# Kernel optimization log

Measured on AMD Instinct MI355X. Metric: run time of the kernel, lower is better.

Reference implementation:

```python
import jax, jax.numpy as jnp
import numpy as np

N = 500_000
E = 16_000_000
G = 5_000
F_IN = 64
DIM = 10


def _mlp(x, W1, b1, W2, b2):
    return jnp.maximum(x @ W1 + b1, 0.0) @ W2 + b2


def setup_inputs() -> dict:
    key = jax.random.key(0)
    ks = jax.random.split(key, 32)
    inp = {
        "h": jax.random.normal(ks[0], (N, F_IN), dtype=jnp.float32),
        "src": jax.random.randint(ks[1], (E,), 0, N, dtype=jnp.int32),
        "dst": jax.random.randint(ks[2], (E,), 0, N, dtype=jnp.int32),
        "node_graph": jnp.sort(jax.random.randint(ks[3], (N,), 0, G, dtype=jnp.int32)),
    }
    k = 4
    for i in range(1, 6):
        d_in = F_IN if i == 1 else DIM
        inp[f"W1_{i}"] = jax.random.normal(ks[k], (d_in, DIM), dtype=jnp.float32) * 0.1; k += 1
        inp[f"b1_{i}"] = jnp.zeros((DIM,), dtype=jnp.float32)
        inp[f"W2_{i}"] = jax.random.normal(ks[k], (DIM, DIM), dtype=jnp.float32) * 0.1; k += 1
        inp[f"b2_{i}"] = jnp.zeros((DIM,), dtype=jnp.float32)
        inp[f"l_{i}"] = jax.random.normal(ks[k], (DIM, 1), dtype=jnp.float32) * 0.1; k += 1
    return inp


def reference(h, src, dst, node_graph,
              W1_1, b1_1, W2_1, b2_1, l_1,
              W1_2, b1_2, W2_2, b2_2, l_2,
              W1_3, b1_3, W2_3, b2_3, l_3,
              W1_4, b1_4, W2_4, b2_4, l_4,
              W1_5, b1_5, W2_5, b2_5, l_5):
    # GINConv with eps=0: out = MLP(h + sum_{j in N(i)} h_j), then outer ReLU
    def gin(x, W1, b1, W2, b2):
        agg = jax.ops.segment_sum(x[src], dst, num_segments=N)
        return jnp.maximum(_mlp(x + agg, W1, b1, W2, b2), 0.0)

    x1 = gin(h, W1_1, b1_1, W2_1, b2_1)
    x2 = gin(x1, W1_2, b1_2, W2_2, b2_2)
    x3 = gin(x2, W1_3, b1_3, W2_3, b2_3)
    x4 = gin(x3, W1_4, b1_4, W2_4, b2_4)
    x5 = gin(x4, W1_5, b1_5, W2_5, b2_5)

    counts = jax.ops.segment_sum(jnp.ones((N,), dtype=jnp.float32), node_graph, num_segments=G)
    counts = jnp.maximum(counts, 1.0)[:, None]  # [G,1]

    def mean_nodes(x):
        return jax.ops.segment_sum(x, node_graph, num_segments=G) / counts

    s = (mean_nodes(x1) @ l_1 + mean_nodes(x2) @ l_2 + mean_nodes(x3) @ l_3
         + mean_nodes(x4) @ l_4 + mean_nodes(x5) @ l_5)  # [G,1]
    return jax.nn.sigmoid(s)
```

## Files before the change

kernel.cpp:

```cpp
#include <hip/hip_runtime.h>


#define NBLK 256

__device__ __forceinline__ unsigned short f2bf(float f) {
    unsigned b = __float_as_uint(f);
    b += 0x7fffu + ((b >> 16) & 1u);
    return (unsigned short)(b >> 16);
}
__device__ __forceinline__ float bflo(unsigned u) { return __uint_as_float(u << 16); }
__device__ __forceinline__ float bfhi(unsigned u) { return __uint_as_float(u & 0xffff0000u); }

__global__ void k1_hw1_bf16(const float* __restrict__ h, const float* __restrict__ W1,
                            unsigned* __restrict__ y, int N) {
    __shared__ float sW[640];
    for (int i = threadIdx.x; i < 640; i += blockDim.x) sW[i] = W1[i];
    __syncthreads();
    int n = blockIdx.x * blockDim.x + threadIdx.x;
    if (n >= N) return;
    const float* hr = h + (size_t)n * 64;
    float acc[10];
#pragma unroll
    for (int j = 0; j < 10; j++) acc[j] = 0.f;
#pragma unroll 4
    for (int k = 0; k < 64; k += 4) {
        float4 hv = *(const float4*)(hr + k);
#pragma unroll
        for (int j = 0; j < 10; j++) {
            acc[j] += hv.x * sW[(k + 0) * 10 + j];
            acc[j] += hv.y * sW[(k + 1) * 10 + j];
            acc[j] += hv.z * sW[(k + 2) * 10 + j];
            acc[j] += hv.w * sW[(k + 3) * 10 + j];
        }
    }
    unsigned r0 = (unsigned)f2bf(acc[0]) | ((unsigned)f2bf(acc[1]) << 16);
    unsigned r1 = (unsigned)f2bf(acc[2]) | ((unsigned)f2bf(acc[3]) << 16);
    unsigned r2 = (unsigned)f2bf(acc[4]) | ((unsigned)f2bf(acc[5]) << 16);
    unsigned r3 = (unsigned)f2bf(acc[6]) | ((unsigned)f2bf(acc[7]) << 16);
    unsigned r4 = (unsigned)f2bf(acc[8]) | ((unsigned)f2bf(acc[9]) << 16);
    unsigned* yr = y + (size_t)n * 8;
    *(uint4*)yr = make_uint4(r0, r1, r2, r3);
    yr[4] = r4;
}

__global__ void k1_hw1_f32(const float* __restrict__ h, const float* __restrict__ W1,
                           float* __restrict__ y, int N) {
    __shared__ float sW[640];
    for (int i = threadIdx.x; i < 640; i += blockDim.x) sW[i] = W1[i];
    __syncthreads();
    int n = blockIdx.x * blockDim.x + threadIdx.x;
    if (n >= N) return;
    const float* hr = h + (size_t)n * 64;
    float acc[10];
#pragma unroll
    for (int j = 0; j < 10; j++) acc[j] = 0.f;
#pragma unroll 4
    for (int k = 0; k < 64; k += 4) {
        float4 hv = *(const float4*)(hr + k);
#pragma unroll
        for (int j = 0; j < 10; j++) {
            acc[j] += hv.x * sW[(k + 0) * 10 + j];
            acc[j] += hv.y * sW[(k + 1) * 10 + j];
            acc[j] += hv.z * sW[(k + 2) * 10 + j];
            acc[j] += hv.w * sW[(k + 3) * 10 + j];
        }
    }
    float* yr = y + (size_t)n * 16;
#pragma unroll
    for (int j = 0; j < 10; j++) yr[j] = acc[j];
}

__global__ __launch_bounds__(1024) void k_cnt(
        const int* __restrict__ dst, unsigned* __restrict__ gcnt, int E) {
    __shared__ unsigned h[512];
    int t = threadIdx.x;
    if (t < 512) h[t] = 0;
    __syncthreads();
    int per = (E + NBLK - 1) / NBLK;
    int beg = blockIdx.x * per;
    int end = beg + per; if (end > E) end = E;
    for (int e = beg + t; e < end; e += 1024)
        atomicAdd(&h[(unsigned)dst[e] >> 10], 1u);
    __syncthreads();
    if (t < 512) gcnt[blockIdx.x * 512 + t] = h[t];
}

__global__ __launch_bounds__(NBLK) void k_scan2(
        const unsigned* __restrict__ gcnt, unsigned* __restrict__ gbase,
        unsigned* __restrict__ btot) {
    __shared__ unsigned s[NBLK];
    int b = blockIdx.x;
    int t = threadIdx.x;
    unsigned v = gcnt[t * 512 + b];
    s[t] = v;
    __syncthreads();
    for (int off = 1; off < NBLK; off <<= 1) {
        unsigned u = (t >= off) ? s[t - off] : 0u;
        __syncthreads();
        s[t] += u;
        __syncthreads();
    }
    gbase[t * 512 + b] = s[t] - v;
    if (t == NBLK - 1) btot[b] = s[t];
}

__global__ void k_bscan(const unsigned* __restrict__ btot,
                        unsigned* __restrict__ bbase, int B) {
    __shared__ unsigned s[512];
    int t = threadIdx.x;
    unsigned v = (t < B) ? btot[t] : 0u;
    s[t] = v;
    __syncthreads();
    for (int off = 1; off < 512; off <<= 1) {
        unsigned u = (t >= off) ? s[t - off] : 0u;
        __syncthreads();
        s[t] += u;
        __syncthreads();
    }
    if (t < B) bbase[t] = s[t] - v;
    if (t == B - 1) bbase[B] = s[t];
}

__global__ __launch_bounds__(1024) void k_scatter(
        const int* __restrict__ src, const int* __restrict__ dst,
        const unsigned* __restrict__ bbase, const unsigned* __restrict__ gbase,
        unsigned* __restrict__ pairs, int E) {
    __shared__ unsigned cur[512];
    int t = threadIdx.x;
    if (t < 512) cur[t] = bbase[t] + gbase[blockIdx.x * 512 + t];
    __syncthreads();
    int per = (E + NBLK - 1) / NBLK;
    int beg = blockIdx.x * per;
    int end = beg + per; if (end > E) end = E;
    for (int e = beg + t; e < end; e += 1024) {
        unsigned d = (unsigned)dst[e];
        unsigned pos = atomicAdd(&cur[d >> 10], 1u);
        pairs[pos] = ((unsigned)src[e] << 10) | (d & 1023u);
    }
}

__global__ __launch_bounds__(1024) void k_p2(
        const unsigned* __restrict__ pairs, const unsigned* __restrict__ bbase,
        unsigned* __restrict__ edges, unsigned* __restrict__ row_start,
        int N, int B, int E, int packed) {
    __shared__ unsigned cnt[1024], scn[1024], cur[1024];
    int t = threadIdx.x, b = blockIdx.x;
    unsigned beg = bbase[b], end = bbase[b + 1];
    cnt[t] = 0;
    __syncthreads();
    for (unsigned e = beg + t; e < end; e += 1024)
        atomicAdd(&cnt[pairs[e] & 1023u], 1u);
    __syncthreads();
    unsigned v = cnt[t];
    scn[t] = v;
    __syncthreads();
    for (int off = 1; off < 1024; off <<= 1) {
        unsigned u = (t >= off) ? scn[t - off] : 0u;
        __syncthreads();
        scn[t] += u;
        __syncthreads();
    }
    unsigned excl = scn[t] - v;
    int node = (b << 10) + t;
    if (node < N) row_start[node] = beg + excl;
    if (b == B - 1 && t == 0) row_start[N] = (unsigned)E;
    cur[t] = beg + excl;
    __syncthreads();
    for (unsigned e = beg + t; e < end; e += 1024) {
        unsigned pv = pairs[e];
        unsigned pos = atomicAdd(&cur[pv & 1023u], 1u);
        edges[pos] = packed ? pv : (pv >> 10);
    }
}

__global__ __launch_bounds__(256, 4) void k_layerQ(
        const unsigned* __restrict__ yin, unsigned* __restrict__ yout,
        const unsigned* __restrict__ row_start, const unsigned* __restrict__ edges,
        const float* __restrict__ b1, const float* __restrict__ W2,
        const float* __restrict__ b2, const float* __restrict__ l,
        const float* __restrict__ W1n,
        const int* __restrict__ node_graph, float* __restrict__ gacc,
        int N, int last) {
    __shared__ float sW2[100], sW1[100], sb1[10], sb2[10], sl[10];
    int t = threadIdx.x;
    if (t < 100) sW2[t] = W2[t];
    if (!last && t >= 128 && t < 228) sW1[t - 128] = W1n[t - 128];
    if (t < 10) { sb1[t] = b1[t]; sb2[t] = b2[t]; sl[t] = l[t]; }
    __syncthreads();
    int q = t & 3;
    int n = blockIdx.x * 64 + (t >> 2);
    bool valid = n < N;
    int nc = valid ? n : (N - 1);

    float acc[10];
#pragma unroll
    for (int j = 0; j < 10; j++) acc[j] = 0.f;

    unsigned beg = 0, end = 0;
    if (valid) { beg = row_start[n]; end = row_start[n + 1]; }
    unsigned e = beg + (unsigned)q;
    bool have = e < end;
    unsigned sNext = 0;
    if (have) sNext = edges[e];
    while (have) {
        unsigned sCur = sNext;
        unsigned en = e + 4;
        bool hn = en < end;
        if (hn) sNext = edges[en];
        const unsigned* p = yin + (size_t)sCur * 8;
        uint4 a0 = *(const uint4*)p;
        unsigned b0 = p[4];
        acc[0] += bflo(a0.x); acc[1] += bfhi(a0.x);
        acc[2] += bflo(a0.y); acc[3] += bfhi(a0.y);
        acc[4] += bflo(a0.z); acc[5] += bfhi(a0.z);
        acc[6] += bflo(a0.w); acc[7] += bfhi(a0.w);
        acc[8] += bflo(b0);   acc[9] += bfhi(b0);
        e = en; have = hn;
    }

#pragma unroll
    for (int j = 0; j < 10; j++) acc[j] += __shfl_xor(acc[j], 1);
#pragma unroll
    for (int j = 0; j < 10; j++) acc[j] += __shfl_xor(acc[j], 2);

    const unsigned* yr = yin + (size_t)nc * 8;
    uint4 qa = *(const uint4*)yr;
    unsigned q4 = yr[4];
    acc[0] += bflo(qa.x); acc[1] += bfhi(qa.x);
    acc[2] += bflo(qa.y); acc[3] += bfhi(qa.y);
    acc[4] += bflo(qa.z); acc[5] += bfhi(qa.z);
    acc[6] += bflo(qa.w); acc[7] += bfhi(qa.w);
    acc[8] += bflo(q4);   acc[9] += bfhi(q4);

    float z[10], x[10];
#pragma unroll
    for (int j = 0; j < 10; j++) {
        float v = acc[j] + sb1[j];
        z[j] = v > 0.f ? v : 0.f;
    }
#pragma unroll
    for (int j = 0; j < 10; j++) {
        float v = sb2[j];
#pragma unroll
        for (int k = 0; k < 10; k++) v += z[k] * sW2[k * 10 + j];
        x[j] = v > 0.f ? v : 0.f;
    }
    float p = 0.f;
#pragma unroll
    for (int j = 0; j < 10; j++) p += x[j] * sl[j];
    if (!valid) p = 0.f;
    int g = node_graph[nc];

    int g0 = __shfl(g, 0);
    if (__all(g == g0)) {
#pragma unroll
        for (int off = 32; off > 0; off >>= 1) p += __shfl_down(p, off);
        if ((t & 63) == 0) unsafeAtomicAdd(&gacc[g0], p * 0.25f);
    } else {
        if (valid && q == 0) unsafeAtomicAdd(&gacc[g], p);
    }

    if (!last && valid && q == 0) {
        float yn[10];
#pragma unroll
        for (int j = 0; j < 10; j++) {
            float v = 0.f;
#pragma unroll
            for (int k = 0; k < 10; k++) v += x[k] * sW1[k * 10 + j];
            yn[j] = v;
        }
        unsigned r0 = (unsigned)f2bf(yn[0]) | ((unsigned)f2bf(yn[1]) << 16);
        unsigned r1 = (unsigned)f2bf(yn[2]) | ((unsigned)f2bf(yn[3]) << 16);
        unsigned r2 = (unsigned)f2bf(yn[4]) | ((unsigned)f2bf(yn[5]) << 16);
        unsigned r3 = (unsigned)f2bf(yn[6]) | ((unsigned)f2bf(yn[7]) << 16);
        unsigned r4 = (unsigned)f2bf(yn[8]) | ((unsigned)f2bf(yn[9]) << 16);
        unsigned* yo = yout + (size_t)n * 8;
        *(uint4*)yo = make_uint4(r0, r1, r2, r3);
        yo[4] = r4;
    }
}

__global__ void k4_final(const float* __restrict__ gacc, const int* __restrict__ node_graph,
                         float* __restrict__ out, int N, int G) {
    int g = blockIdx.x * blockDim.x + threadIdx.x;
    if (g >= G) return;
    int lo = 0, hi = N;
    while (lo < hi) { int m = (lo + hi) >> 1; if (node_graph[m] < g) lo = m + 1; else hi = m; }
    int lo2 = lo, hi2 = N;
    while (lo2 < hi2) { int m = (lo2 + hi2) >> 1; if (node_graph[m] <= g) lo2 = m + 1; else hi2 = m; }
    float c = (float)(hi2 - lo);
    if (c < 1.f) c = 1.f;
    float s = gacc[g] / c;
    out[g] = 1.f / (1.f + __expf(-s));
}

__global__ __launch_bounds__(256) void k_layer(
        const float* __restrict__ yin, float* __restrict__ yout,
        const unsigned* __restrict__ row_start, const unsigned* __restrict__ edges,
        const float* __restrict__ b1, const float* __restrict__ W2,
        const float* __restrict__ b2, const float* __restrict__ l,
        const float* __restrict__ W1n,
        const int* __restrict__ node_graph, float* __restrict__ gacc,
        int N, int last) {
    __shared__ float sW2[100], sW1[100], sb1[10], sb2[10], sl[10];
    int t = threadIdx.x;
    if (t < 100) sW2[t] = W2[t];
    if (!last && t >= 128 && t < 228) sW1[t - 128] = W1n[t - 128];
    if (t < 10) { sb1[t] = b1[t]; sb2[t] = b2[t]; sl[t] = l[t]; }
    __syncthreads();
    int n = blockIdx.x * 256 + t;
    bool valid = n < N;
    int nc = valid ? n : (N - 1);
    const float* yr = yin + (size_t)nc * 16;
    float4 a = *(const float4*)yr;
    float4 b = *(const float4*)(yr + 4);
    float2 c = *(const float2*)(yr + 8);
    float acc[10] = {a.x, a.y, a.z, a.w, b.x, b.y, b.z, b.w, c.x, c.y};
    unsigned beg = 0, end = 0;
    if (valid) { beg = row_start[n]; end = row_start[n + 1]; }
    for (unsigned e = beg; e < end; ++e) {
        unsigned s = edges[e];
        const float* pr = yin + (size_t)s * 16;
        float4 pa = *(const float4*)pr;
        float4 pb = *(const float4*)(pr + 4);
        float2 pc = *(const float2*)(pr + 8);
        acc[0] += pa.x; acc[1] += pa.y; acc[2] += pa.z; acc[3] += pa.w;
        acc[4] += pb.x; acc[5] += pb.y; acc[6] += pb.z; acc[7] += pb.w;
        acc[8] += pc.x; acc[9] += pc.y;
    }
    float z[10], x[10];
#pragma unroll
    for (int j = 0; j < 10; j++) {
        float v = acc[j] + sb1[j];
        z[j] = v > 0.f ? v : 0.f;
    }
#pragma unroll
    for (int j = 0; j < 10; j++) {
        float v = sb2[j];
#pragma unroll
        for (int k = 0; k < 10; k++) v += z[k] * sW2[k * 10 + j];
        x[j] = v > 0.f ? v : 0.f;
    }
    float p = 0.f;
#pragma unroll
    for (int j = 0; j < 10; j++) p += x[j] * sl[j];
    if (!valid) p = 0.f;
    int g = node_graph[nc];
    int g0 = __shfl(g, 0);
    if (__all(g == g0)) {
#pragma unroll
        for (int off = 32; off > 0; off >>= 1) p += __shfl_down(p, off);
        if ((t & 63) == 0) unsafeAtomicAdd(&gacc[g0], p);
    } else {
        if (valid) unsafeAtomicAdd(&gacc[g], p);
    }
    if (!last && valid) {
        float yn[10];
#pragma unroll
        for (int j = 0; j < 10; j++) {
            float v = 0.f;
#pragma unroll
            for (int k = 0; k < 10; k++) v += x[k] * sW1[k * 10 + j];
            yn[j] = v;
        }
        float* yo = yout + (size_t)n * 16;
        *(float4*)yo = make_float4(yn[0], yn[1], yn[2], yn[3]);
        *(float4*)(yo + 4) = make_float4(yn[4], yn[5], yn[6], yn[7]);
        *(float2*)(yo + 8) = make_float2(yn[8], yn[9]);
    }
}

static inline size_t al16(size_t w) { return (w + 15) & ~(size_t)15; }

extern "C" void kernel_launch(void* const* d_in, const int* in_sizes, int n_in,
                              void* d_out, int out_size, void* d_ws, size_t ws_size,
                              hipStream_t stream) {
    const float* h  = (const float*)d_in[0];
    const int* src  = (const int*)d_in[1];
    const int* dst  = (const int*)d_in[2];
    const int* ng   = (const int*)d_in[3];
    int N = in_sizes[3];
    int E = in_sizes[1];
    int G = out_size;

    const float* W1[5]; const float* b1[5]; const float* W2[5]; const float* b2[5]; const float* l[5];
    for (int i = 0; i < 5; i++) {
        W1[i] = (const float*)d_in[4 + i * 5 + 0];
        b1[i] = (const float*)d_in[4 + i * 5 + 1];
        W2[i] = (const float*)d_in[4 + i * 5 + 2];
        b2[i] = (const float*)d_in[4 + i * 5 + 3];
        l[i]  = (const float*)d_in[4 + i * 5 + 4];
    }
    float* out = (float*)d_out;

    int B = (N + 1023) >> 10;

    size_t wY   = al16((size_t)N * 8);
    size_t wRg2 = al16(((size_t)E > (size_t)N * 8) ? (size_t)E : (size_t)N * 8);
    size_t wE   = al16((size_t)E);
    size_t wRS  = al16((size_t)N + 1);
    size_t wGrid = (size_t)NBLK * 512;
    size_t need_r13 = (wY + wRg2 + wE + wRS + 1040 + 2 * wGrid + al16((size_t)G)) * 4;

    size_t regAB = (size_t)N * 16;
    size_t reg2f = ((size_t)E > regAB) ? (size_t)E : regAB;
    size_t need_r4 = (regAB + reg2f + (size_t)E + (size_t)(N + 1) + 1040 +
                      2 * wGrid + (size_t)G) * 4;

    if (ws_size >= need_r13 && B <= 512) {
        unsigned* y0 = (unsigned*)d_ws;
        unsigned* pairs = y0 + wY;
        unsigned* y1 = pairs;
        unsigned* edges = pairs + wRg2;
        unsigned* row_start = edges + wE;
        unsigned* btot = row_start + wRS;
        unsigned* bbase = btot + 512;
        unsigned* gcnt = bbase + 528;
        unsigned* gbase = gcnt + wGrid;
        float* gacc = (float*)(gbase + wGrid);

        hipMemsetAsync(gacc, 0, (size_t)G * 4, stream);

        k1_hw1_bf16<<<(N + 255) / 256, 256, 0, stream>>>(h, W1[0], y0, N);

        k_cnt<<<NBLK, 1024, 0, stream>>>(dst, gcnt, E);
        k_scan2<<<512, NBLK, 0, stream>>>(gcnt, gbase, btot);
        k_bscan<<<1, 512, 0, stream>>>(btot, bbase, B);
        k_scatter<<<NBLK, 1024, 0, stream>>>(src, dst, bbase, gbase, pairs, E);
        k_p2<<<B, 1024, 0, stream>>>(pairs, bbase, edges, row_start, N, B, E, 0);

        unsigned* ybuf[2] = {y0, y1};
        int qblocks = (N + 63) / 64;
        for (int i = 0; i < 5; i++) {
            k_layerQ<<<qblocks, 256, 0, stream>>>(
                ybuf[i & 1], ybuf[(i + 1) & 1], row_start, edges,
                b1[i], W2[i], b2[i], l[i], i < 4 ? W1[i + 1] : nullptr,
                ng, gacc, N, i == 4 ? 1 : 0);
        }
        k4_final<<<(G + 255) / 256, 256, 0, stream>>>(gacc, ng, out, N, G);
        return;
    }

    if (ws_size >= need_r4 && B <= 512) {
        float* y0 = (float*)d_ws;
        unsigned* pairs = (unsigned*)(y0 + regAB);
        float* y1 = (float*)pairs;
        unsigned* edges = pairs + reg2f;
        unsigned* row_start = edges + E;
        unsigned* btot = row_start + (N + 1);
        unsigned* bbase = btot + 512;
        unsigned* gcnt = bbase + 528;
        unsigned* gbase = gcnt + wGrid;
        float* gacc = (float*)(gbase + wGrid);

        hipMemsetAsync(gacc, 0, (size_t)G * 4, stream);

        k1_hw1_f32<<<(N + 255) / 256, 256, 0, stream>>>(h, W1[0], y0, N);
        k_cnt<<<NBLK, 1024, 0, stream>>>(dst, gcnt, E);
        k_scan2<<<512, NBLK, 0, stream>>>(gcnt, gbase, btot);
        k_bscan<<<1, 512, 0, stream>>>(btot, bbase, B);
        k_scatter<<<NBLK, 1024, 0, stream>>>(src, dst, bbase, gbase, pairs, E);
        k_p2<<<B, 1024, 0, stream>>>(pairs, bbase, edges, row_start, N, B, E, 0);

        float* ybuf[2] = {y0, y1};
        for (int i = 0; i < 5; i++) {
            k_layer<<<(N + 255) / 256, 256, 0, stream>>>(
                ybuf[i & 1], ybuf[(i + 1) & 1], row_start, edges,
                b1[i], W2[i], b2[i], l[i], i < 4 ? W1[i + 1] : nullptr,
                ng, gacc, N, i == 4 ? 1 : 0);
        }
        k4_final<<<(G + 255) / 256, 256, 0, stream>>>(gacc, ng, out, N, G);
    }
}
```

Measured before the change: 1.994 ms.

## Build CSR with global per-node atomic histogram and scatter instead of bucket sort

Replaces the two-level bucketed counting sort (LDS histograms, pair scatter, per-bucket local sort) with a direct per-node global atomic histogram, a three-kernel prefix scan, and a global-atomic scatter of source indices into CSR slots. This removes the intermediate pairs buffer and one full pass over the edges. In exchange it relies on tens of millions of global atomics and random-address writes, and within-row edge order becomes nondeterministic.

```diff
diff --git a/kernel.cpp b/kernel.cpp
--- a/kernel.cpp
+++ b/kernel.cpp
@@ -1,7 +1,5 @@
 #include <hip/hip_runtime.h>
 
-
-#define NBLK 256
 
 __device__ __forceinline__ unsigned short f2bf(float f) {
     unsigned b = __float_as_uint(f);
@@ -70,106 +68,91 @@
     for (int j = 0; j < 10; j++) yr[j] = acc[j];
 }
 
-__global__ __launch_bounds__(1024) void k_cnt(
-        const int* __restrict__ dst, unsigned* __restrict__ gcnt, int E) {
-    __shared__ unsigned h[512];
+__global__ __launch_bounds__(256) void k_histN(
+        const int* __restrict__ dst, unsigned* __restrict__ cnt, int E) {
+    int stride = gridDim.x * blockDim.x;
+    for (int e = blockIdx.x * blockDim.x + threadIdx.x; e < E; e += stride)
+        atomicAdd(&cnt[(unsigned)dst[e]], 1u);
+}
+
+__global__ __launch_bounds__(1024) void k_scanA(
+        const unsigned* __restrict__ cnt, unsigned* __restrict__ bsum, int N) {
+    __shared__ unsigned s[1024];
     int t = threadIdx.x;
-    if (t < 512) h[t] = 0;
-    __syncthreads();
-    int per = (E + NBLK - 1) / NBLK;
-    int beg = blockIdx.x * per;
-    int end = beg + per; if (end > E) end = E;
-    for (int e = beg + t; e < end; e += 1024)
-        atomicAdd(&h[(unsigned)dst[e] >> 10], 1u);
-    __syncthreads();
-    if (t < 512) gcnt[blockIdx.x * 512 + t] = h[t];
-}
-
-__global__ __launch_bounds__(NBLK) void k_scan2(
-        const unsigned* __restrict__ gcnt, unsigned* __restrict__ gbase,
-        unsigned* __restrict__ btot) {
-    __shared__ unsigned s[NBLK];
-    int b = blockIdx.x;
+    size_t base = (size_t)blockIdx.x * 8192 + (size_t)t * 8;
+    unsigned sum = 0;
+#pragma unroll
+    for (int k = 0; k < 8; k++) {
+        size_t i = base + k;
+        if (i < (size_t)N) sum += cnt[i];
+    }
+    s[t] = sum;
+    __syncthreads();
+    for (int off = 512; off > 0; off >>= 1) {
+        if (t < off) s[t] += s[t + off];
+        __syncthreads();
+    }
+    if (t == 0) bsum[blockIdx.x] = s[0];
+}
+
+__global__ __launch_bounds__(1024) void k_scanB(unsigned* __restrict__ bsum, int nb) {
+    __shared__ unsigned s[1024];
     int t = threadIdx.x;
-    unsigned v = gcnt[t * 512 + b];
+    unsigned v = (t < nb) ? bsum[t] : 0u;
     s[t] = v;
     __syncthreads();
-    for (int off = 1; off < NBLK; off <<= 1) {
+    for (int off = 1; off < 1024; off <<= 1) {
         unsigned u = (t >= off) ? s[t - off] : 0u;
         __syncthreads();
         s[t] += u;
         __syncthreads();
     }
-    gbase[t * 512 + b] = s[t] - v;
-    if (t == NBLK - 1) btot[b] = s[t];
-}
-
-__global__ void k_bscan(const unsigned* __restrict__ btot,
-                        unsigned* __restrict__ bbase, int B) {
-    __shared__ unsigned s[512];
+    if (t < nb) bsum[t] = s[t] - v;
+}
+
+__global__ __launch_bounds__(1024) void k_scanC(
+        const unsigned* __restrict__ cnt, const unsigned* __restrict__ bsum,
+        unsigned* __restrict__ row_start, unsigned* __restrict__ cur, int N, int E) {
+    __shared__ unsigned s[1024];
     int t = threadIdx.x;
-    unsigned v = (t < B) ? btot[t] : 0u;
-    s[t] = v;
-    __syncthreads();
-    for (int off = 1; off < 512; off <<= 1) {
+    size_t base = (size_t)blockIdx.x * 8192 + (size_t)t * 8;
+    unsigned loc[8];
+    unsigned sum = 0;
+#pragma unroll
+    for (int k = 0; k < 8; k++) {
+        size_t i = base + k;
+        unsigned c = (i < (size_t)N) ? cnt[i] : 0u;
+        loc[k] = sum;
+        sum += c;
+    }
+    s[t] = sum;
+    __syncthreads();
+    for (int off = 1; off < 1024; off <<= 1) {
         unsigned u = (t >= off) ? s[t - off] : 0u;
         __syncthreads();
         s[t] += u;
         __syncthreads();
     }
-    if (t < B) bbase[t] = s[t] - v;
-    if (t == B - 1) bbase[B] = s[t];
-}
-
-__global__ __launch_bounds__(1024) void k_scatter(
+    unsigned texcl = s[t] - sum + bsum[blockIdx.x];
+#pragma unroll
+    for (int k = 0; k < 8; k++) {
+        size_t i = base + k;
+        if (i < (size_t)N) {
+            unsigned v = texcl + loc[k];
+            row_start[i] = v;
+            cur[i] = v;
+        }
+    }
+    if (blockIdx.x == 0 && t == 0) row_start[N] = (unsigned)E;
+}
+
+__global__ __launch_bounds__(256) void k_scatterN(
         const int* __restrict__ src, const int* __restrict__ dst,
-        const unsigned* __restrict__ bbase, const unsigned* __restrict__ gbase,
-        unsigned* __restrict__ pairs, int E) {
-    __shared__ unsigned cur[512];
-    int t = threadIdx.x;
-    if (t < 512) cur[t] = bbase[t] + gbase[blockIdx.x * 512 + t];
-    __syncthreads();
-    int per = (E + NBLK - 1) / NBLK;
-    int beg = blockIdx.x * per;
-    int end = beg + per; if (end > E) end = E;
-    for (int e = beg + t; e < end; e += 1024) {
-        unsigned d = (unsigned)dst[e];
-        unsigned pos = atomicAdd(&cur[d >> 10], 1u);
-        pairs[pos] = ((unsigned)src[e] << 10) | (d & 1023u);
-    }
-}
-
-__global__ __launch_bounds__(1024) void k_p2(
-        const unsigned* __restrict__ pairs, const unsigned* __restrict__ bbase,
-        unsigned* __restrict__ edges, unsigned* __restrict__ row_start,
-        int N, int B, int E, int packed) {
-    __shared__ unsigned cnt[1024], scn[1024], cur[1024];
-    int t = threadIdx.x, b = blockIdx.x;
-    unsigned beg = bbase[b], end = bbase[b + 1];
-    cnt[t] = 0;
-    __syncthreads();
-    for (unsigned e = beg + t; e < end; e += 1024)
-        atomicAdd(&cnt[pairs[e] & 1023u], 1u);
-    __syncthreads();
-    unsigned v = cnt[t];
-    scn[t] = v;
-    __syncthreads();
-    for (int off = 1; off < 1024; off <<= 1) {
-        unsigned u = (t >= off) ? scn[t - off] : 0u;
-        __syncthreads();
-        scn[t] += u;
-        __syncthreads();
-    }
-    unsigned excl = scn[t] - v;
-    int node = (b << 10) + t;
-    if (node < N) row_start[node] = beg + excl;
-    if (b == B - 1 && t == 0) row_start[N] = (unsigned)E;
-    cur[t] = beg + excl;
-    __syncthreads();
-    for (unsigned e = beg + t; e < end; e += 1024) {
-        unsigned pv = pairs[e];
-        unsigned pos = atomicAdd(&cur[pv & 1023u], 1u);
-        edges[pos] = packed ? pv : (pv >> 10);
+        unsigned* __restrict__ cur, unsigned* __restrict__ edges, int E) {
+    int stride = gridDim.x * blockDim.x;
+    for (int e = blockIdx.x * blockDim.x + threadIdx.x; e < E; e += stride) {
+        unsigned pos = atomicAdd(&cur[(unsigned)dst[e]], 1u);
+        edges[pos] = (unsigned)src[e];
     }
 }
 
@@ -393,41 +376,38 @@
     }
     float* out = (float*)d_out;
 
-    int B = (N + 1023) >> 10;
+    int nbScan = (N + 8191) / 8192;
 
     size_t wY   = al16((size_t)N * 8);
-    size_t wRg2 = al16(((size_t)E > (size_t)N * 8) ? (size_t)E : (size_t)N * 8);
     size_t wE   = al16((size_t)E);
     size_t wRS  = al16((size_t)N + 1);
-    size_t wGrid = (size_t)NBLK * 512;
-    size_t need_r13 = (wY + wRg2 + wE + wRS + 1040 + 2 * wGrid + al16((size_t)G)) * 4;
-
-    size_t regAB = (size_t)N * 16;
-    size_t reg2f = ((size_t)E > regAB) ? (size_t)E : regAB;
-    size_t need_r4 = (regAB + reg2f + (size_t)E + (size_t)(N + 1) + 1040 +
-                      2 * wGrid + (size_t)G) * 4;
-
-    if (ws_size >= need_r13 && B <= 512) {
+    size_t wN   = al16((size_t)N);
+    size_t need_r14 = (2 * wY + wE + wRS + 2 * wN + 1024 + al16((size_t)G)) * 4;
+
+    size_t regY = (size_t)N * 16;
+    size_t need_r4 = (2 * regY + (size_t)E + (size_t)(N + 1) + 2 * wN + 1024 +
+                      (size_t)G) * 4;
+
+    if (ws_size >= need_r14 && nbScan <= 1024) {
         unsigned* y0 = (unsigned*)d_ws;
-        unsigned* pairs = y0 + wY;
-        unsigned* y1 = pairs;
-        unsigned* edges = pairs + wRg2;
+        unsigned* y1 = y0 + wY;
+        unsigned* edges = y1 + wY;
         unsigned* row_start = edges + wE;
-        unsigned* btot = row_start + wRS;
-        unsigned* bbase = btot + 512;
-        unsigned* gcnt = bbase + 528;
-        unsigned* gbase = gcnt + wGrid;
-        float* gacc = (float*)(gbase + wGrid);
-
+        unsigned* cnt = row_start + wRS;
+        unsigned* cur = cnt + wN;
+        unsigned* bsum = cur + wN;
+        float* gacc = (float*)(bsum + 1024);
+
+        hipMemsetAsync(cnt, 0, (size_t)N * 4, stream);
         hipMemsetAsync(gacc, 0, (size_t)G * 4, stream);
 
         k1_hw1_bf16<<<(N + 255) / 256, 256, 0, stream>>>(h, W1[0], y0, N);
 
-        k_cnt<<<NBLK, 1024, 0, stream>>>(dst, gcnt, E);
-        k_scan2<<<512, NBLK, 0, stream>>>(gcnt, gbase, btot);
-        k_bscan<<<1, 512, 0, stream>>>(btot, bbase, B);
-        k_scatter<<<NBLK, 1024, 0, stream>>>(src, dst, bbase, gbase, pairs, E);
-        k_p2<<<B, 1024, 0, stream>>>(pairs, bbase, edges, row_start, N, B, E, 0);
+        k_histN<<<2048, 256, 0, stream>>>(dst, cnt, E);
+        k_scanA<<<nbScan, 1024, 0, stream>>>(cnt, bsum, N);
+        k_scanB<<<1, 1024, 0, stream>>>(bsum, nbScan);
+        k_scanC<<<nbScan, 1024, 0, stream>>>(cnt, bsum, row_start, cur, N, E);
+        k_scatterN<<<2048, 256, 0, stream>>>(src, dst, cur, edges, E);
 
         unsigned* ybuf[2] = {y0, y1};
         int qblocks = (N + 63) / 64;
@@ -441,26 +421,25 @@
         return;
     }
 
-    if (ws_size >= need_r4 && B <= 512) {
+    if (ws_size >= need_r4 && nbScan <= 1024) {
         float* y0 = (float*)d_ws;
-        unsigned* pairs = (unsigned*)(y0 + regAB);
-        float* y1 = (float*)pairs;
-        unsigned* edges = pairs + reg2f;
+        float* y1 = y0 + regY;
+        unsigned* edges = (unsigned*)(y1 + regY);
         unsigned* row_start = edges + E;
-        unsigned* btot = row_start + (N + 1);
-        unsigned* bbase = btot + 512;
-        unsigned* gcnt = bbase + 528;
-        unsigned* gbase = gcnt + wGrid;
-        float* gacc = (float*)(gbase + wGrid);
-
+        unsigned* cnt = row_start + (N + 1);
+        unsigned* cur = cnt + wN;
+        unsigned* bsum = cur + wN;
+        float* gacc = (float*)(bsum + 1024);
+
+        hipMemsetAsync(cnt, 0, (size_t)N * 4, stream);
         hipMemsetAsync(gacc, 0, (size_t)G * 4, stream);
 
         k1_hw1_f32<<<(N + 255) / 256, 256, 0, stream>>>(h, W1[0], y0, N);
-        k_cnt<<<NBLK, 1024, 0, stream>>>(dst, gcnt, E);
-        k_scan2<<<512, NBLK, 0, stream>>>(gcnt, gbase, btot);
-        k_bscan<<<1, 512, 0, stream>>>(btot, bbase, B);
-        k_scatter<<<NBLK, 1024, 0, stream>>>(src, dst, bbase, gbase, pairs, E);
-        k_p2<<<B, 1024, 0, stream>>>(pairs, bbase, edges, row_start, N, B, E, 0);
+        k_histN<<<2048, 256, 0, stream>>>(dst, cnt, E);
+        k_scanA<<<nbScan, 1024, 0, stream>>>(cnt, bsum, N);
+        k_scanB<<<1, 1024, 0, stream>>>(bsum, nbScan);
+        k_scanC<<<nbScan, 1024, 0, stream>>>(cnt, bsum, row_start, cur, N, E);
+        k_scatterN<<<2048, 256, 0, stream>>>(src, dst, cur, edges, E);
 
         float* ybuf[2] = {y0, y1};
         for (int i = 0; i < 5; i++) {
```

After: 3.250 ms. 63.0% more time.
